# Kernel optimization log

Measured on AMD Instinct MI355X. Metric: run time of the kernel, lower is better.

The kernel has to match this reference:

```python
import jax, jax.numpy as jnp
import numpy as np

INPUT_DIM, SLOT_DIM, ATT_DIM = 180, 1536, 1536


def layernorm(x, gamma, beta, eps=1e-5):
    mu = jnp.mean(x, axis=-1, keepdims=True)
    var = jnp.var(x, axis=-1, keepdims=True)
    return (x - mu) * jax.lax.rsqrt(var + eps) * gamma + beta


def setup_inputs() -> dict:
    key = jax.random.key(0)
    ks = jax.random.split(key, 4)
    B, I, S = 8, 8192, 64
    x = jax.random.normal(ks[0], (B, I, INPUT_DIM), dtype=jnp.float32)
    slot_latents = jax.random.normal(ks[1], (B, S, SLOT_DIM), dtype=jnp.float32)
    Wq = jax.random.normal(ks[2], (INPUT_DIM, ATT_DIM), dtype=jnp.float32) / np.sqrt(INPUT_DIM)
    Wk = jax.random.normal(ks[3], (SLOT_DIM, ATT_DIM), dtype=jnp.float32) / np.sqrt(SLOT_DIM)
    g1 = jnp.ones((INPUT_DIM,), jnp.float32)
    b1 = jnp.zeros((INPUT_DIM,), jnp.float32)
    g2 = jnp.ones((SLOT_DIM,), jnp.float32)
    b2 = jnp.zeros((SLOT_DIM,), jnp.float32)
    return {"x": x, "slot_latents": slot_latents, "Wq": Wq, "Wk": Wk,
            "g1": g1, "b1": b1, "g2": g2, "b2": b2}


def reference(x, slot_latents, Wq, Wk, g1, b1, g2, b2):
    scale = ATT_DIM ** (-0.5)
    xn = layernorm(x, g1, b1)                      # (B,I,input_dim)
    q = xn @ Wq                                     # (B,I,att_dim)
    k = slot_latents @ Wk                           # (B,S,att_dim)
    dots = jnp.einsum('bid,bsd->bis', q, k) * scale
    w = jax.nn.softmax(dots, axis=2)                # (B,I,S)
    # identical math to (w[...,None] * slots[:,None]).sum(2), fused as matmul
    s = jnp.einsum('bis,bsd->bid', w, slot_latents)  # (B,I,slot_dim)
    s = layernorm(s, g2, b2)
    return (s, w)
```

## Files before the change

kernel.cpp:

```cpp
#include <hip/hip_runtime.h>

#define IDIM 180
#define SDIM 1536
#define NB   8
#define NI   8192
#define NS   64

typedef short bf16x8 __attribute__((ext_vector_type(8)));
typedef float f32x4  __attribute__((ext_vector_type(4)));

__device__ __forceinline__ short f2bf(float x){
  union { float f; unsigned u; } v; v.f = x;
  unsigned r = v.u + 0x7fffu + ((v.u >> 16) & 1u);
  return (short)(r >> 16);
}

__device__ __forceinline__ bf16x8 cvt8(const float* p){
  const float4* p4 = (const float4*)p;
  float4 a = p4[0], b = p4[1];
  bf16x8 r;
  r[0]=f2bf(a.x); r[1]=f2bf(a.y); r[2]=f2bf(a.z); r[3]=f2bf(a.w);
  r[4]=f2bf(b.x); r[5]=f2bf(b.y); r[6]=f2bf(b.z); r[7]=f2bf(b.w);
  return r;
}

__global__ __launch_bounds__(256) void kA(const float* __restrict__ slot,
                                          short* __restrict__ slot_bf,
                                          short* __restrict__ slotT){
  int i = blockIdx.x * 256 + threadIdx.x;
  float v = slot[i];
  short h = f2bf(v);
  slot_bf[i] = h;
  int d  = i % SDIM;
  int bs = i / SDIM;
  int b  = bs >> 6, s = bs & 63;
  slotT[((b * SDIM + d) << 6) + s] = h;
}

__global__ __launch_bounds__(256) void kB(const float* __restrict__ Wq,
                                          const float* __restrict__ Wk,
                                          short* __restrict__ Abf){
  int tn = blockIdx.x;
  int t = threadIdx.x, w = t >> 6, l = t & 63;
  int l15 = l & 15, q = l >> 4;
  int cc = tn * 16 + l15;
  const float* wkrow = Wk + (size_t)cc * SDIM;
  f32x4 acc[3];
  #pragma unroll
  for (int tt = 0; tt < 3; ++tt) acc[tt] = (f32x4){0.f,0.f,0.f,0.f};
  for (int ks = 0; ks < 48; ++ks){
    int d0 = ks * 32 + q * 8;
    bf16x8 bfrag = cvt8(wkrow + d0);
    #pragma unroll
    for (int tt = 0; tt < 3; ++tt){
      int e = (w + 4*tt) * 16 + l15;
      bf16x8 afrag = {0,0,0,0,0,0,0,0};
      if (e < IDIM) afrag = cvt8(Wq + (size_t)e * SDIM + d0);
      acc[tt] = __builtin_amdgcn_mfma_f32_16x16x32_bf16(afrag, bfrag, acc[tt], 0, 0, 0);
    }
  }
  #pragma unroll
  for (int tt = 0; tt < 3; ++tt){
    int tm = w + 4*tt;
    #pragma unroll
    for (int r = 0; r < 4; ++r){
      int e = tm * 16 + q * 4 + r;
      Abf[(size_t)e * SDIM + cc] = f2bf(acc[tt][r]);
    }
  }
}

__global__ __launch_bounds__(256) void kC(const short* __restrict__ Abf,
                                          const short* __restrict__ slot_bf,
                                          short* __restrict__ MT){
  int b = blockIdx.x >> 2, tn = blockIdx.x & 3;
  int t = threadIdx.x, w = t >> 6, l = t & 63;
  int l15 = l & 15, q = l >> 4;
  int s = tn * 16 + l15;
  const short* srow = slot_bf + (size_t)(b * NS + s) * SDIM;
  f32x4 acc[3];
  #pragma unroll
  for (int tt = 0; tt < 3; ++tt) acc[tt] = (f32x4){0.f,0.f,0.f,0.f};
  for (int ks = 0; ks < 48; ++ks){
    int c0 = ks * 32 + q * 8;
    bf16x8 bfrag = *(const bf16x8*)(srow + c0);
    #pragma unroll
    for (int tt = 0; tt < 3; ++tt){
      int e = (w + 4*tt) * 16 + l15;
      bf16x8 afrag = *(const bf16x8*)(Abf + (size_t)e * SDIM + c0);
      acc[tt] = __builtin_amdgcn_mfma_f32_16x16x32_bf16(afrag, bfrag, acc[tt], 0, 0, 0);
    }
  }
  #pragma unroll
  for (int tt = 0; tt < 3; ++tt){
    #pragma unroll
    for (int r = 0; r < 4; ++r){
      int e = (w + 4*tt) * 16 + q * 4 + r;
      MT[(size_t)(b * NS + s) * 192 + e] = f2bf(acc[tt][r]);
    }
  }
}

__global__ __launch_bounds__(256) void kD(const float* __restrict__ x,
                                          const short* __restrict__ slotT,
                                          const short* __restrict__ MT,
                                          const float* __restrict__ g1,
                                          const float* __restrict__ b1,
                                          const float* __restrict__ g2,
                                          const float* __restrict__ b2,
                                          float* __restrict__ outS,
                                          float* __restrict__ outW){
  __shared__ __align__(16) float xs[16 * IDIM];
  __shared__ __align__(16) short xnbf[16 * 192];
  __shared__ __align__(16) float dotsS[16 * 68];
  __shared__ __align__(16) short wbf[16 * 80];
  __shared__ float stats[4][16][2];
  __shared__ float smu[16], srstd[16];

  int t = threadIdx.x;
  int blk = blockIdx.x;
  int b = blk >> 9;
  int i0 = (blk & 511) << 4;
  const float* xp = x + (size_t)(b * NI + i0) * IDIM;

  {
    const float4* src = (const float4*)xp;
    float4* dst = (float4*)xs;
    for (int idx = t; idx < 720; idx += 256) dst[idx] = src[idx];
  }
  __syncthreads();

  {
    int row = t >> 4, j16 = t & 15;
    float vals[12];
    float sum = 0.f, sq = 0.f;
    #pragma unroll
    for (int k = 0; k < 12; ++k){
      int e = j16 + 16 * k;
      float v = (e < IDIM) ? xs[row * IDIM + e] : 0.f;
      vals[k] = v; sum += v; sq += v * v;
    }
    #pragma unroll
    for (int m = 1; m < 16; m <<= 1){ sum += __shfl_xor(sum, m); sq += __shfl_xor(sq, m); }
    float mu  = sum * (1.f / IDIM);
    float var = sq * (1.f / IDIM) - mu * mu;
    float rstd = rsqrtf(var + 1e-5f);
    #pragma unroll
    for (int k = 0; k < 12; ++k){
      int e = j16 + 16 * k;
      float xn = (e < IDIM) ? (vals[k] - mu) * rstd * g1[e] + b1[e] : 0.f;
      xnbf[row * 192 + e] = f2bf(xn);
    }
  }
  __syncthreads();

  int w = t >> 6, l = t & 63, l15 = l & 15, q = l >> 4;

  {
    f32x4 acc = (f32x4){0.f,0.f,0.f,0.f};
    const short* mtb = MT + (size_t)(b * NS + 16 * w + l15) * 192;
    #pragma unroll
    for (int ks = 0; ks < 6; ++ks){
      bf16x8 af = *(const bf16x8*)(xnbf + l15 * 192 + ks * 32 + q * 8);
      bf16x8 bf = *(const bf16x8*)(mtb + ks * 32 + q * 8);
      acc = __builtin_amdgcn_mfma_f32_16x16x32_bf16(af, bf, acc, 0, 0, 0);
    }
    const float scale = 0.025515518153991442f;
    #pragma unroll
    for (int r = 0; r < 4; ++r)
      dotsS[(q * 4 + r) * 68 + 16 * w + l15] = acc[r] * scale;
  }
  __syncthreads();

  {
    int row = t >> 4, j16 = t & 15;
    float d0[4];
    float mx = -1e30f;
    #pragma unroll
    for (int j = 0; j < 4; ++j){ d0[j] = dotsS[row * 68 + j16 + 16 * j]; mx = fmaxf(mx, d0[j]); }
    #pragma unroll
    for (int m = 1; m < 16; m <<= 1) mx = fmaxf(mx, __shfl_xor(mx, m));
    float sum = 0.f;
    #pragma unroll
    for (int j = 0; j < 4; ++j){ d0[j] = __expf(d0[j] - mx); sum += d0[j]; }
    #pragma unroll
    for (int m = 1; m < 16; m <<= 1) sum += __shfl_xor(sum, m);
    float inv = 1.f / sum;
    float* wrow = outW + (size_t)(b * NI + i0 + row) * NS;
    #pragma unroll
    for (int j = 0; j < 4; ++j){
      float wv = d0[j] * inv;
      wrow[j16 + 16 * j] = wv;
      wbf[row * 80 + j16 + 16 * j] = f2bf(wv);
    }
  }
  __syncthreads();

  {
    bf16x8 a0 = *(const bf16x8*)(wbf + l15 * 80 + q * 8);
    bf16x8 a1 = *(const bf16x8*)(wbf + l15 * 80 + 32 + q * 8);
    const short* stb = slotT + ((size_t)b * SDIM) * NS;
    f32x4 acc[24];
    float sum[4] = {0,0,0,0}, sq[4] = {0,0,0,0};
    #pragma unroll
    for (int ct = 0; ct < 24; ++ct){
      int c = w * 384 + ct * 16 + l15;
      const short* col = stb + (size_t)c * NS;
      bf16x8 bf0 = *(const bf16x8*)(col + q * 8);
      bf16x8 bf1 = *(const bf16x8*)(col + 32 + q * 8);
      f32x4 a = (f32x4){0.f,0.f,0.f,0.f};
      a = __builtin_amdgcn_mfma_f32_16x16x32_bf16(a0, bf0, a, 0, 0, 0);
      a = __builtin_amdgcn_mfma_f32_16x16x32_bf16(a1, bf1, a, 0, 0, 0);
      acc[ct] = a;
      #pragma unroll
      for (int r = 0; r < 4; ++r){ sum[r] += a[r]; sq[r] += a[r] * a[r]; }
    }
    #pragma unroll
    for (int m = 1; m < 16; m <<= 1){
      #pragma unroll
      for (int r = 0; r < 4; ++r){
        sum[r] += __shfl_xor(sum[r], m);
        sq[r]  += __shfl_xor(sq[r],  m);
      }
    }
    if (l15 == 0){
      #pragma unroll
      for (int r = 0; r < 4; ++r){
        stats[w][q * 4 + r][0] = sum[r];
        stats[w][q * 4 + r][1] = sq[r];
      }
    }
    __syncthreads();
    if (t < 16){
      float s0 = 0.f, s1 = 0.f;
      #pragma unroll
      for (int ww = 0; ww < 4; ++ww){ s0 += stats[ww][t][0]; s1 += stats[ww][t][1]; }
      float mu  = s0 * (1.f / SDIM);
      float var = s1 * (1.f / SDIM) - mu * mu;
      smu[t] = mu; srstd[t] = rsqrtf(var + 1e-5f);
    }
    __syncthreads();
    float mu[4], rs[4];
    #pragma unroll
    for (int r = 0; r < 4; ++r){ mu[r] = smu[q * 4 + r]; rs[r] = srstd[q * 4 + r]; }
    float* obase = outS + (size_t)(b * NI + i0) * SDIM;
    #pragma unroll
    for (int ct = 0; ct < 24; ++ct){
      int c = w * 384 + ct * 16 + l15;
      float g = g2[c], bb = b2[c];
      float* orow = obase + c;
      #pragma unroll
      for (int r = 0; r < 4; ++r){
        float v = (acc[ct][r] - mu[r]) * rs[r] * g + bb;
        orow[(size_t)(q * 4 + r) * SDIM] = v;
      }
    }
  }
}

extern "C" void kernel_launch(void* const* d_in, const int* in_sizes, int n_in,
                              void* d_out, int out_size, void* d_ws, size_t ws_size,
                              hipStream_t stream){
  const float* x    = (const float*)d_in[0];
  const float* slot = (const float*)d_in[1];
  const float* Wq   = (const float*)d_in[2];
  const float* Wk   = (const float*)d_in[3];
  const float* g1   = (const float*)d_in[4];
  const float* b1   = (const float*)d_in[5];
  const float* g2   = (const float*)d_in[6];
  const float* b2   = (const float*)d_in[7];
  float* outS = (float*)d_out;
  float* outW = outS + (size_t)NB * NI * SDIM;

  short* slot_bf = (short*)d_ws;
  short* slotT   = slot_bf + (size_t)NB * NS * SDIM;
  short* A_bf    = slotT + (size_t)NB * NS * SDIM;
  short* MT      = A_bf + (size_t)192 * SDIM;

  kA<<<(NB * NS * SDIM) / 256, 256, 0, stream>>>(slot, slot_bf, slotT);
  kB<<<96, 256, 0, stream>>>(Wq, Wk, A_bf);
  kC<<<32, 256, 0, stream>>>(A_bf, slot_bf, MT);
  kD<<<(NB * NI) / 16, 256, 0, stream>>>(x, slotT, MT, g1, b1, g2, b2, outS, outW);
}
```

Measured before the change: 662.6 us.

## Recompute second matmul instead of holding accumulators; nontemporal output stores; tiled slot transpose

The final kernel no longer keeps 24 MFMA accumulator tiles live across the layernorm statistics pass. It recomputes the small two-MFMA products in the normalisation pass, which cuts register pressure and may raise occupancy, at the cost of doubling that matmul and its slotT loads. The large fp32 outputs (normalised slots and attention weights) are now written with nontemporal stores to reduce cache pollution. The slot conversion/transpose kernel is also rewritten to stage through a shared-memory tile so that writes to the transposed layout are coalesced.

```diff
diff --git a/kernel.cpp b/kernel.cpp
--- a/kernel.cpp
+++ b/kernel.cpp
@@ -27,14 +27,35 @@
 __global__ __launch_bounds__(256) void kA(const float* __restrict__ slot,
                                           short* __restrict__ slot_bf,
                                           short* __restrict__ slotT){
-  int i = blockIdx.x * 256 + threadIdx.x;
-  float v = slot[i];
-  short h = f2bf(v);
-  slot_bf[i] = h;
-  int d  = i % SDIM;
-  int bs = i / SDIM;
-  int b  = bs >> 6, s = bs & 63;
-  slotT[((b * SDIM + d) << 6) + s] = h;
+  __shared__ short tile[64 * 66];
+  int b  = blockIdx.x / 24;
+  int d0 = (blockIdx.x % 24) * 64;
+  int t  = threadIdx.x;
+  {
+    int s  = t >> 2;
+    int dd = (t & 3) * 16;
+    const float* src = slot + (size_t)(b * NS + s) * SDIM + d0 + dd;
+    short* dst_bf = slot_bf + (size_t)(b * NS + s) * SDIM + d0 + dd;
+    #pragma unroll
+    for (int k = 0; k < 4; ++k){
+      float4 v = ((const float4*)src)[k];
+      short h0 = f2bf(v.x), h1 = f2bf(v.y), h2 = f2bf(v.z), h3 = f2bf(v.w);
+      dst_bf[4*k+0] = h0; dst_bf[4*k+1] = h1; dst_bf[4*k+2] = h2; dst_bf[4*k+3] = h3;
+      tile[s * 66 + dd + 4*k + 0] = h0;
+      tile[s * 66 + dd + 4*k + 1] = h1;
+      tile[s * 66 + dd + 4*k + 2] = h2;
+      tile[s * 66 + dd + 4*k + 3] = h3;
+    }
+  }
+  __syncthreads();
+  {
+    int d  = t >> 2;
+    int s0 = (t & 3) * 16;
+    short* dst = slotT + ((size_t)(b * SDIM + d0 + d) << 6) + s0;
+    #pragma unroll
+    for (int k = 0; k < 16; ++k)
+      dst[k] = tile[(s0 + k) * 66 + d];
+  }
 }
 
 __global__ __launch_bounds__(256) void kB(const float* __restrict__ Wq,
@@ -190,7 +211,7 @@
     #pragma unroll
     for (int j = 0; j < 4; ++j){
       float wv = d0[j] * inv;
-      wrow[j16 + 16 * j] = wv;
+      __builtin_nontemporal_store(wv, wrow + j16 + 16 * j);
       wbf[row * 80 + j16 + 16 * j] = f2bf(wv);
     }
   }
@@ -200,9 +221,8 @@
     bf16x8 a0 = *(const bf16x8*)(wbf + l15 * 80 + q * 8);
     bf16x8 a1 = *(const bf16x8*)(wbf + l15 * 80 + 32 + q * 8);
     const short* stb = slotT + ((size_t)b * SDIM) * NS;
-    f32x4 acc[24];
+
     float sum[4] = {0,0,0,0}, sq[4] = {0,0,0,0};
-    #pragma unroll
     for (int ct = 0; ct < 24; ++ct){
       int c = w * 384 + ct * 16 + l15;
       const short* col = stb + (size_t)c * NS;
@@ -211,7 +231,6 @@
       f32x4 a = (f32x4){0.f,0.f,0.f,0.f};
       a = __builtin_amdgcn_mfma_f32_16x16x32_bf16(a0, bf0, a, 0, 0, 0);
       a = __builtin_amdgcn_mfma_f32_16x16x32_bf16(a1, bf1, a, 0, 0, 0);
-      acc[ct] = a;
       #pragma unroll
       for (int r = 0; r < 4; ++r){ sum[r] += a[r]; sq[r] += a[r] * a[r]; }
     }
@@ -243,16 +262,22 @@
     float mu[4], rs[4];
     #pragma unroll
     for (int r = 0; r < 4; ++r){ mu[r] = smu[q * 4 + r]; rs[r] = srstd[q * 4 + r]; }
+
     float* obase = outS + (size_t)(b * NI + i0) * SDIM;
-    #pragma unroll
     for (int ct = 0; ct < 24; ++ct){
       int c = w * 384 + ct * 16 + l15;
+      const short* col = stb + (size_t)c * NS;
+      bf16x8 bf0 = *(const bf16x8*)(col + q * 8);
+      bf16x8 bf1 = *(const bf16x8*)(col + 32 + q * 8);
+      f32x4 a = (f32x4){0.f,0.f,0.f,0.f};
+      a = __builtin_amdgcn_mfma_f32_16x16x32_bf16(a0, bf0, a, 0, 0, 0);
+      a = __builtin_amdgcn_mfma_f32_16x16x32_bf16(a1, bf1, a, 0, 0, 0);
       float g = g2[c], bb = b2[c];
       float* orow = obase + c;
       #pragma unroll
       for (int r = 0; r < 4; ++r){
-        float v = (acc[ct][r] - mu[r]) * rs[r] * g + bb;
-        orow[(size_t)(q * 4 + r) * SDIM] = v;
+        float v = (a[r] - mu[r]) * rs[r] * g + bb;
+        __builtin_nontemporal_store(v, orow + (size_t)(q * 4 + r) * SDIM);
       }
     }
   }
@@ -277,7 +302,7 @@
   short* A_bf    = slotT + (size_t)NB * NS * SDIM;
   short* MT      = A_bf + (size_t)192 * SDIM;
 
-  kA<<<(NB * NS * SDIM) / 256, 256, 0, stream>>>(slot, slot_bf, slotT);
+  kA<<<192, 256, 0, stream>>>(slot, slot_bf, slotT);
   kB<<<96, 256, 0, stream>>>(Wq, Wk, A_bf);
   kC<<<32, 256, 0, stream>>>(A_bf, slot_bf, MT);
   kD<<<(NB * NI) / 16, 256, 0, stream>>>(x, slotT, MT, g1, b1, g2, b2, outS, outW);
```

Result: slower. 733.3 us (+10.7%).
